# Performance work log

Measured on AMD Instinct MI355X. Metric: run time of the kernel, lower is better.

## Reference

```python
import jax, jax.numpy as jnp
import numpy as np

N_NODES = 100000


def setup_inputs() -> dict:
    key = jax.random.key(0)
    ks = jax.random.split(key, 6)
    x = jax.random.normal(ks[0], (N_NODES, 3), dtype=jnp.float32)
    edge_index = jax.random.randint(ks[1], (2, 1600000), 0, N_NODES, dtype=jnp.int32)
    W1 = jax.random.normal(ks[2], (6, 64), dtype=jnp.float32) * 0.2
    b1 = jnp.zeros((64,), dtype=jnp.float32)
    W2 = jax.random.normal(ks[3], (67, 128), dtype=jnp.float32) * 0.1
    b2 = jnp.zeros((128,), dtype=jnp.float32)
    Wc = jax.random.normal(ks[4], (128, 5), dtype=jnp.float32) * 0.1
    bc = jnp.zeros((5,), dtype=jnp.float32)
    return {"x": x, "edge_index": edge_index, "W1": W1, "b1": b1,
            "W2": W2, "b2": b2, "Wc": Wc, "bc": bc}


def _pointnet_conv(h, rel, src, dst, W, b, n):
    # gather neighbor features, MLP on [h_j, pos_j - pos_i], max-aggregate per node
    msg = jnp.concatenate([h[src], rel], axis=-1) @ W + b  # [E, out]
    agg = jax.ops.segment_max(msg, dst, num_segments=n)    # [N, out]
    return jax.nn.relu(agg)  # relu also maps -inf (isolated nodes) to 0


def reference(x, edge_index, W1, b1, W2, b2, Wc, bc):
    src, dst = edge_index[0], edge_index[1]
    pos = x  # forward uses data.x for both x and pos
    rel = pos[src] - pos[dst]                       # [E, 3]
    h = _pointnet_conv(x, rel, src, dst, W1, b1, N_NODES)   # [N, 64]
    h = _pointnet_conv(h, rel, src, dst, W2, b2, N_NODES)   # [N, 128]
    logits = h @ Wc + bc                            # [N, 5]
    return jax.nn.log_softmax(logits, axis=-1)
```

## Files before the change

### kernel.cpp

```cpp
#include <hip/hip_runtime.h>
#include <cstdint>

#define CAP 56
#define NBITS 7
#define BINSZ 128
#define TILE_E 4096
#define SCANN 1024
#define EPT (TILE_E/256)

typedef _Float16 h2 __attribute__((ext_vector_type(2)));
typedef _Float16 h4 __attribute__((ext_vector_type(4)));
typedef _Float16 h8 __attribute__((ext_vector_type(8)));
typedef float f32x4 __attribute__((ext_vector_type(4)));

static __device__ inline h8 pkmax8(h8 a, h8 b) {
#if __has_builtin(__builtin_elementwise_max)
    return __builtin_elementwise_max(a, b);
#else
    h8 r;
    #pragma unroll
    for (int i = 0; i < 8; i += 2) {
        h2 aa = { a[i], a[i+1] }, bb = { b[i], b[i+1] }, rr;
        asm("v_pk_max_f16 %0, %1, %2" : "=v"(rr) : "v"(aa), "v"(bb));
        r[i] = rr.x; r[i+1] = rr.y;
    }
    return r;
#endif
}

__global__ __launch_bounds__(256) void bin_kernel(
    const float* __restrict__ x, const int* __restrict__ ei,
    float4* __restrict__ xp, int* __restrict__ words_out,
    int* __restrict__ tsc, int N, int E)
{
    for (int n = blockIdx.x * 256 + threadIdx.x; n < N; n += gridDim.x * 256)
        xp[n] = make_float4(x[n*3], x[n*3+1], x[n*3+2], 0.f);

    __shared__ int hist[SCANN];
    __shared__ int sc[SCANN];
    __shared__ int lofs[SCANN];
    __shared__ int words[TILE_E];
    int t = threadIdx.x;
    int tile = blockIdx.x;
    for (int i = t; i < SCANN; i += 256) { hist[i] = 0; lofs[i] = 0; }
    __syncthreads();
    int e0 = tile * TILE_E;
    int s[EPT], d[EPT];
    #pragma unroll
    for (int i = 0; i < EPT; ++i) {
        int e = e0 + t + i * 256;
        bool ok = e < E;
        s[i] = ok ? ei[e] : 0;
        d[i] = ok ? ei[E + e] : -1;
        if (ok) atomicAdd(&hist[d[i] >> NBITS], 1);
    }
    __syncthreads();
    for (int i = t; i < SCANN; i += 256) sc[i] = hist[i];
    __syncthreads();
    for (int off = 1; off < SCANN; off <<= 1) {
        int v[4];
        #pragma unroll
        for (int j = 0; j < 4; ++j) {
            int i = t + j * 256;
            v[j] = (i >= off) ? sc[i - off] : 0;
        }
        __syncthreads();
        #pragma unroll
        for (int j = 0; j < 4; ++j) sc[t + j * 256] += v[j];
        __syncthreads();
    }
    #pragma unroll
    for (int i = 0; i < EPT; ++i) {
        if (d[i] >= 0) {
            int b = d[i] >> NBITS;
            int p = atomicAdd(&lofs[b], 1);
            int slot = (sc[b] - hist[b]) + p;
            words[slot] = s[i] | ((d[i] & (BINSZ - 1)) << 17);
        }
    }
    __syncthreads();
    int* wo = words_out + tile * TILE_E;
    for (int i = t; i < TILE_E; i += 256) wo[i] = words[i];
    int* to = tsc + tile * SCANN;
    for (int i = t; i < SCANN; i += 256) to[i] = sc[i];
}

__global__ __launch_bounds__(256) void scatter2_kernel(
    const int* __restrict__ words, const int* __restrict__ tsc,
    int* __restrict__ cursor, int* __restrict__ bucket,
    int N, int ntiles)
{
    __shared__ int cur[BINSZ];
    __shared__ int lbuck[BINSZ * CAP];
    int t = threadIdx.x;
    int b = blockIdx.x;
    for (int i = t; i < BINSZ; i += 256) cur[i] = 0;
    __syncthreads();
    for (int tt = t; tt < ntiles; tt += 256) {
        int base = tt * SCANN;
        int s0 = (b > 0) ? tsc[base + b - 1] : 0;
        int s1 = tsc[base + b];
        const int* wp = words + tt * TILE_E;
        for (int i = s0; i < s1; ++i) {
            int w = wp[i];
            int p = atomicAdd(&cur[w >> 17], 1);
            if (p < CAP) lbuck[(w >> 17) * CAP + p] = w & 0x1FFFF;
        }
    }
    __syncthreads();
    int nbase = b * BINSZ;
    for (int dl = t; dl < BINSZ; dl += 256) {
        int n = nbase + dl;
        if (n >= N) continue;
        int c = min(cur[dl], CAP);
        int e = (c + 7) & ~7;
        int s0 = (c > 0) ? lbuck[dl * CAP] : 0;
        for (int p = c; p < e; ++p) lbuck[dl * CAP + p] = s0;
        cursor[n] = c;
    }
    __syncthreads();
    int4* dst = (int4*)(bucket + (size_t)nbase * CAP);
    const int4* srcv = (const int4*)lbuck;
    for (int i = t; i < BINSZ * CAP / 4; i += 256) dst[i] = srcv[i];
}

__global__ __launch_bounds__(256) void agg1_gemm_kernel(
    const float4* __restrict__ xp, const int* __restrict__ cursor,
    const int* __restrict__ bucket, const float* __restrict__ W1,
    const float* __restrict__ b1, const float* __restrict__ W2,
    const float* __restrict__ b2, _Float16* __restrict__ u2h, int N)
{
    __shared__ _Float16 h1[64 * 72];
    __shared__ _Float16 w2t[128 * 72];
    int tid = threadIdx.x;
    int n0  = blockIdx.x * 64;
    int sub = tid & 15;
    int ng  = tid >> 4;

    {
        const float4* W2v4 = (const float4*)W2;
        #pragma unroll
        for (int it = 0; it < 8; ++it) {
            int idx = tid + it * 256;
            int k = idx >> 5, c = (idx & 31) * 4;
            float4 w = W2v4[idx];
            w2t[(c+0)*72 + k] = (_Float16)w.x;
            w2t[(c+1)*72 + k] = (_Float16)w.y;
            w2t[(c+2)*72 + k] = (_Float16)w.z;
            w2t[(c+3)*72 + k] = (_Float16)w.w;
        }
    }

    float4 q0 = ((const float4*)(W1 + 0*64))[sub];
    float4 q1 = ((const float4*)(W1 + 1*64))[sub];
    float4 q2 = ((const float4*)(W1 + 2*64))[sub];
    float4 t0 = ((const float4*)(W1 + 3*64))[sub];
    float4 t1 = ((const float4*)(W1 + 4*64))[sub];
    float4 t2 = ((const float4*)(W1 + 5*64))[sub];
    float4 c0 = make_float4(q0.x+t0.x, q0.y+t0.y, q0.z+t0.z, q0.w+t0.w);
    float4 c1 = make_float4(q1.x+t1.x, q1.y+t1.y, q1.z+t1.z, q1.w+t1.w);
    float4 c2 = make_float4(q2.x+t2.x, q2.y+t2.y, q2.z+t2.z, q2.w+t2.w);
    float4 bb = ((const float4*)b1)[sub];

    #pragma unroll
    for (int pass = 0; pass < 4; ++pass) {
        int nl = pass * 16 + ng;
        int n  = n0 + nl;
        float4 m = make_float4(-3e38f, -3e38f, -3e38f, -3e38f);
        int cnt = 0;
        if (n < N) {
            cnt = cursor[n];
            int rounds = (cnt + 7) & ~7;
            const int4* brow4 = (const int4*)(bucket + (size_t)n * CAP);
            int4 ia = brow4[0], ib = brow4[1];
            for (int j0 = 0; j0 < rounds; j0 += 8) {
                int4 na = brow4[(j0 >> 2) + 2];
                int4 nb = brow4[(j0 >> 2) + 3];
                float4 xs[8];
                xs[0] = xp[ia.x]; xs[1] = xp[ia.y]; xs[2] = xp[ia.z]; xs[3] = xp[ia.w];
                xs[4] = xp[ib.x]; xs[5] = xp[ib.y]; xs[6] = xp[ib.z]; xs[7] = xp[ib.w];
                #pragma unroll
                for (int u = 0; u < 8; ++u) {
                    float4 v;
                    v.x = fmaf(xs[u].x, c0.x, fmaf(xs[u].y, c1.x, xs[u].z * c2.x));
                    v.y = fmaf(xs[u].x, c0.y, fmaf(xs[u].y, c1.y, xs[u].z * c2.y));
                    v.z = fmaf(xs[u].x, c0.z, fmaf(xs[u].y, c1.z, xs[u].z * c2.z));
                    v.w = fmaf(xs[u].x, c0.w, fmaf(xs[u].y, c1.w, xs[u].z * c2.w));
                    m.x = fmaxf(m.x, v.x); m.y = fmaxf(m.y, v.y);
                    m.z = fmaxf(m.z, v.z); m.w = fmaxf(m.w, v.w);
                }
                ia = na; ib = nb;
            }
        }
        float4 xd = (n < N) ? xp[n] : make_float4(0.f, 0.f, 0.f, 0.f);
        float v0 = (cnt > 0) ? fmaxf(m.x + bb.x - (xd.x*t0.x + xd.y*t1.x + xd.z*t2.x), 0.f) : 0.f;
        float v1 = (cnt > 0) ? fmaxf(m.y + bb.y - (xd.x*t0.y + xd.y*t1.y + xd.z*t2.y), 0.f) : 0.f;
        float v2 = (cnt > 0) ? fmaxf(m.z + bb.z - (xd.x*t0.z + xd.y*t1.z + xd.z*t2.z), 0.f) : 0.f;
        float v3 = (cnt > 0) ? fmaxf(m.w + bb.w - (xd.x*t0.w + xd.y*t1.w + xd.z*t2.w), 0.f) : 0.f;
        h4 hv;
        hv.x = (_Float16)v0; hv.y = (_Float16)v1;
        hv.z = (_Float16)v2; hv.w = (_Float16)v3;
        *(h4*)&h1[nl * 72 + 4 * sub] = hv;
    }
    __syncthreads();

    int l   = tid & 63;
    int wv  = tid >> 6;
    int r16 = l & 15;
    int g4  = l >> 4;

    f32x4 acc[8];
    #pragma unroll
    for (int ct = 0; ct < 8; ++ct) acc[ct] = (f32x4){0.f, 0.f, 0.f, 0.f};

    h8 a0 = *(const h8*)&h1[(16*wv + r16) * 72 +      8*g4];
    h8 a1 = *(const h8*)&h1[(16*wv + r16) * 72 + 32 + 8*g4];
    #pragma unroll
    for (int ct = 0; ct < 8; ++ct) {
        h8 b0  = *(const h8*)&w2t[(16*ct + r16) * 72 +      8*g4];
        h8 b1f = *(const h8*)&w2t[(16*ct + r16) * 72 + 32 + 8*g4];
        acc[ct] = __builtin_amdgcn_mfma_f32_16x16x32_f16(a0, b0,  acc[ct], 0, 0, 0);
        acc[ct] = __builtin_amdgcn_mfma_f32_16x16x32_f16(a1, b1f, acc[ct], 0, 0, 0);
    }

    float bbv[8], wxv[8], wyv[8], wzv[8];
    #pragma unroll
    for (int ct = 0; ct < 8; ++ct) {
        int col = 16*ct + r16;
        bbv[ct] = b2[col];
        wxv[ct] = W2[64*128 + col];
        wyv[ct] = W2[65*128 + col];
        wzv[ct] = W2[66*128 + col];
    }
    #pragma unroll
    for (int r = 0; r < 4; ++r) {
        int n = n0 + 16*wv + 4*g4 + r;
        if (n < N) {
            float4 xd = xp[n];
            _Float16* orow = u2h + (size_t)n * 128 + r16;
            #pragma unroll
            for (int ct = 0; ct < 8; ++ct) {
                float v = acc[ct][r] + bbv[ct]
                        + xd.x * wxv[ct] + xd.y * wyv[ct] + xd.z * wzv[ct];
                orow[16*ct] = (_Float16)v;
            }
        }
    }
}

__global__ __launch_bounds__(256) void agg2_head_kernel(
    const float* __restrict__ x, const int* __restrict__ cursor,
    const int* __restrict__ bucket, const float* __restrict__ W2,
    const h8* __restrict__ u2v, const float* __restrict__ Wc,
    const float* __restrict__ bc, float* __restrict__ out, int N)
{
    int gid = blockIdx.x * 256 + threadIdx.x;
    int n   = gid >> 4;
    int sub = threadIdx.x & 15;
    if (n >= N) return;
    int cnt = cursor[n];
    int nr = (cnt + 7) >> 3;
    const int4* brow4 = (const int4*)(bucket + (size_t)n * CAP);
    const _Float16 NEG = (_Float16)(-60000.0f);
    h8 hm = { NEG, NEG, NEG, NEG, NEG, NEG, NEG, NEG };
    if (nr > 0) {
        int4 ia = brow4[0], ib = brow4[1];
        h8 v0 = u2v[(size_t)ia.x * 16 + sub];
        h8 v1 = u2v[(size_t)ia.y * 16 + sub];
        h8 v2 = u2v[(size_t)ia.z * 16 + sub];
        h8 v3 = u2v[(size_t)ia.w * 16 + sub];
        h8 v4 = u2v[(size_t)ib.x * 16 + sub];
        h8 v5 = u2v[(size_t)ib.y * 16 + sub];
        h8 v6 = u2v[(size_t)ib.z * 16 + sub];
        h8 v7 = u2v[(size_t)ib.w * 16 + sub];
        int4 na = brow4[2], nb = brow4[3];
        #pragma unroll 2
        for (int r = 1; r < nr; ++r) {
            h8 w0 = u2v[(size_t)na.x * 16 + sub];
            h8 w1 = u2v[(size_t)na.y * 16 + sub];
            h8 w2_ = u2v[(size_t)na.z * 16 + sub];
            h8 w3 = u2v[(size_t)na.w * 16 + sub];
            h8 w4 = u2v[(size_t)nb.x * 16 + sub];
            h8 w5 = u2v[(size_t)nb.y * 16 + sub];
            h8 w6 = u2v[(size_t)nb.z * 16 + sub];
            h8 w7 = u2v[(size_t)nb.w * 16 + sub];
            na = brow4[2*r + 2]; nb = brow4[2*r + 3];
            hm = pkmax8(hm, v0); hm = pkmax8(hm, v1);
            hm = pkmax8(hm, v2); hm = pkmax8(hm, v3);
            hm = pkmax8(hm, v4); hm = pkmax8(hm, v5);
            hm = pkmax8(hm, v6); hm = pkmax8(hm, v7);
            v0 = w0; v1 = w1; v2 = w2_; v3 = w3;
            v4 = w4; v5 = w5; v6 = w6; v7 = w7;
        }
        hm = pkmax8(hm, v0); hm = pkmax8(hm, v1);
        hm = pkmax8(hm, v2); hm = pkmax8(hm, v3);
        hm = pkmax8(hm, v4); hm = pkmax8(hm, v5);
        hm = pkmax8(hm, v6); hm = pkmax8(hm, v7);
    }
    const float4* W2v = (const float4*)W2;
    float4 wa0 = W2v[64*32 + sub*2], wa1 = W2v[64*32 + sub*2 + 1];
    float4 wb0 = W2v[65*32 + sub*2], wb1 = W2v[65*32 + sub*2 + 1];
    float4 wc0 = W2v[66*32 + sub*2], wc1 = W2v[66*32 + sub*2 + 1];
    float x0 = x[n*3], x1 = x[n*3+1], x2 = x[n*3+2];
    float hh[8];
    hh[0] = (cnt > 0) ? fmaxf((float)hm[0] - (x0*wa0.x + x1*wb0.x + x2*wc0.x), 0.f) : 0.f;
    hh[1] = (cnt > 0) ? fmaxf((float)hm[1] - (x0*wa0.y + x1*wb0.y + x2*wc0.y), 0.f) : 0.f;
    hh[2] = (cnt > 0) ? fmaxf((float)hm[2] - (x0*wa0.z + x1*wb0.z + x2*wc0.z), 0.f) : 0.f;
    hh[3] = (cnt > 0) ? fmaxf((float)hm[3] - (x0*wa0.w + x1*wb0.w + x2*wc0.w), 0.f) : 0.f;
    hh[4] = (cnt > 0) ? fmaxf((float)hm[4] - (x0*wa1.x + x1*wb1.x + x2*wc1.x), 0.f) : 0.f;
    hh[5] = (cnt > 0) ? fmaxf((float)hm[5] - (x0*wa1.y + x1*wb1.y + x2*wc1.y), 0.f) : 0.f;
    hh[6] = (cnt > 0) ? fmaxf((float)hm[6] - (x0*wa1.z + x1*wb1.z + x2*wc1.z), 0.f) : 0.f;
    hh[7] = (cnt > 0) ? fmaxf((float)hm[7] - (x0*wa1.w + x1*wb1.w + x2*wc1.w), 0.f) : 0.f;

    int g = sub * 8;
    float l0 = 0.f, l1 = 0.f, l2 = 0.f, l3 = 0.f, l4 = 0.f;
    #pragma unroll
    for (int k = 0; k < 8; ++k) {
        l0 = fmaf(hh[k], Wc[(g+k)*5+0], l0);
        l1 = fmaf(hh[k], Wc[(g+k)*5+1], l1);
        l2 = fmaf(hh[k], Wc[(g+k)*5+2], l2);
        l3 = fmaf(hh[k], Wc[(g+k)*5+3], l3);
        l4 = fmaf(hh[k], Wc[(g+k)*5+4], l4);
    }
    #pragma unroll
    for (int off = 8; off > 0; off >>= 1) {
        l0 += __shfl_xor(l0, off);
        l1 += __shfl_xor(l1, off);
        l2 += __shfl_xor(l2, off);
        l3 += __shfl_xor(l3, off);
        l4 += __shfl_xor(l4, off);
    }
    l0 += bc[0]; l1 += bc[1]; l2 += bc[2]; l3 += bc[3]; l4 += bc[4];
    float mx  = fmaxf(fmaxf(fmaxf(l0, l1), fmaxf(l2, l3)), l4);
    float s   = expf(l0-mx) + expf(l1-mx) + expf(l2-mx) + expf(l3-mx) + expf(l4-mx);
    float lse = mx + logf(s);
    if (sub < 5) {
        float v = (sub == 0) ? l0 : (sub == 1) ? l1 : (sub == 2) ? l2
                : (sub == 3) ? l3 : l4;
        out[n*5 + sub] = v - lse;
    }
}

extern "C" void kernel_launch(void* const* d_in, const int* in_sizes, int n_in,
                              void* d_out, int out_size, void* d_ws, size_t ws_size,
                              hipStream_t stream)
{
    const float* x  = (const float*)d_in[0];
    const int*   ei = (const int*)d_in[1];
    const float* W1 = (const float*)d_in[2];
    const float* b1 = (const float*)d_in[3];
    const float* W2 = (const float*)d_in[4];
    const float* b2 = (const float*)d_in[5];
    const float* Wc = (const float*)d_in[6];
    const float* bc = (const float*)d_in[7];
    float* out = (float*)d_out;

    int N = in_sizes[0] / 3;
    int E = in_sizes[1] / 2;
    int nbins  = (N + BINSZ - 1) / BINSZ;
    int ntiles = (E + TILE_E - 1) / TILE_E;

    char* ws = (char*)d_ws;
    _Float16* u2h   = (_Float16*)(ws);
    float4* xp      = (float4*)(ws + 25600000);
    int*    words   = (int*)   (ws + 27200000);
    int*    tsc     = (int*)   (ws + 33700000);
    int*    bucket  = (int*)   (ws + 36100000);
    int*    cursor  = (int*)   (ws + 58600000);

    bin_kernel<<<ntiles, 256, 0, stream>>>(x, ei, xp, words, tsc, N, E);
    scatter2_kernel<<<nbins, 256, 0, stream>>>(words, tsc, cursor, bucket,
                                               N, ntiles);
    agg1_gemm_kernel<<<(N + 63) / 64, 256, 0, stream>>>(
        xp, cursor, bucket, W1, b1, W2, b2, u2h, N);
    agg2_head_kernel<<<(N * 16 + 255) / 256, 256, 0, stream>>>(
        x, cursor, bucket, W2, (const h8*)u2h, Wc, bc, out, N);
}
```

Baseline: 211.7 us.

## Fuse bucket scatter into layer-1 aggregation kernel using shared-memory neighbor lists

Merges the scatter kernel that builds per-node neighbor buckets with the layer-1 aggregation/GEMM kernel. Each 64-node block now scans its 128-node bin's word segments, keeps only the half it owns, builds the neighbor lists in LDS, writes them out for layer 2, and reads indices directly from LDS for layer-1 aggregation. This drops a kernel launch and the global re-read of bucket/cursor, but every bin's word segments are now scanned twice (once per half-block), and LDS use per block grows, which may lower occupancy.

```diff
diff --git a/kernel.cpp b/kernel.cpp
--- a/kernel.cpp
+++ b/kernel.cpp
@@ -85,57 +85,23 @@
     for (int i = t; i < SCANN; i += 256) to[i] = sc[i];
 }
 
-__global__ __launch_bounds__(256) void scatter2_kernel(
-    const int* __restrict__ words, const int* __restrict__ tsc,
-    int* __restrict__ cursor, int* __restrict__ bucket,
+__global__ __launch_bounds__(256) void scat_agg1_kernel(
+    const float4* __restrict__ xp, const int* __restrict__ words,
+    const int* __restrict__ tsc, const float* __restrict__ W1,
+    const float* __restrict__ b1, const float* __restrict__ W2,
+    const float* __restrict__ b2, int* __restrict__ cursor,
+    int* __restrict__ bucket, _Float16* __restrict__ u2h,
     int N, int ntiles)
 {
-    __shared__ int cur[BINSZ];
-    __shared__ int lbuck[BINSZ * CAP];
-    int t = threadIdx.x;
-    int b = blockIdx.x;
-    for (int i = t; i < BINSZ; i += 256) cur[i] = 0;
-    __syncthreads();
-    for (int tt = t; tt < ntiles; tt += 256) {
-        int base = tt * SCANN;
-        int s0 = (b > 0) ? tsc[base + b - 1] : 0;
-        int s1 = tsc[base + b];
-        const int* wp = words + tt * TILE_E;
-        for (int i = s0; i < s1; ++i) {
-            int w = wp[i];
-            int p = atomicAdd(&cur[w >> 17], 1);
-            if (p < CAP) lbuck[(w >> 17) * CAP + p] = w & 0x1FFFF;
-        }
-    }
-    __syncthreads();
-    int nbase = b * BINSZ;
-    for (int dl = t; dl < BINSZ; dl += 256) {
-        int n = nbase + dl;
-        if (n >= N) continue;
-        int c = min(cur[dl], CAP);
-        int e = (c + 7) & ~7;
-        int s0 = (c > 0) ? lbuck[dl * CAP] : 0;
-        for (int p = c; p < e; ++p) lbuck[dl * CAP + p] = s0;
-        cursor[n] = c;
-    }
-    __syncthreads();
-    int4* dst = (int4*)(bucket + (size_t)nbase * CAP);
-    const int4* srcv = (const int4*)lbuck;
-    for (int i = t; i < BINSZ * CAP / 4; i += 256) dst[i] = srcv[i];
-}
-
-__global__ __launch_bounds__(256) void agg1_gemm_kernel(
-    const float4* __restrict__ xp, const int* __restrict__ cursor,
-    const int* __restrict__ bucket, const float* __restrict__ W1,
-    const float* __restrict__ b1, const float* __restrict__ W2,
-    const float* __restrict__ b2, _Float16* __restrict__ u2h, int N)
-{
+    __shared__ int cur[64];
+    __shared__ int lbuck[64 * CAP];
+    __shared__ _Float16 w2t[128 * 72];
     __shared__ _Float16 h1[64 * 72];
-    __shared__ _Float16 w2t[128 * 72];
     int tid = threadIdx.x;
-    int n0  = blockIdx.x * 64;
-    int sub = tid & 15;
-    int ng  = tid >> 4;
+    int blk = blockIdx.x;
+    int b   = blk >> 1;
+    int hf  = blk & 1;
+    int n0  = blk * 64;
 
     {
         const float4* W2v4 = (const float4*)W2;
@@ -150,7 +116,45 @@
             w2t[(c+3)*72 + k] = (_Float16)w.w;
         }
     }
-
+    if (tid < 64) cur[tid] = 0;
+    __syncthreads();
+
+    for (int tt = tid; tt < ntiles; tt += 256) {
+        int base = tt * SCANN;
+        int s0 = (b > 0) ? tsc[base + b - 1] : 0;
+        int s1 = tsc[base + b];
+        const int* wp = words + tt * TILE_E;
+        for (int i = s0; i < s1; ++i) {
+            int w = wp[i];
+            int dbin = w >> 17;
+            if ((dbin >> 6) == hf) {
+                int p = atomicAdd(&cur[dbin & 63], 1);
+                if (p < CAP) lbuck[(dbin & 63) * CAP + p] = w & 0x1FFFF;
+            }
+        }
+    }
+    __syncthreads();
+    if (tid < 64) {
+        int dl = tid;
+        int n = n0 + dl;
+        if (n < N) {
+            int c = min(cur[dl], CAP);
+            cur[dl] = c;
+            int e = (c + 7) & ~7;
+            int s0 = (c > 0) ? lbuck[dl * CAP] : 0;
+            for (int p = c; p < e; ++p) lbuck[dl * CAP + p] = s0;
+            cursor[n] = c;
+        }
+    }
+    __syncthreads();
+    {
+        int4* dst = (int4*)(bucket + (size_t)n0 * CAP);
+        const int4* srcv = (const int4*)lbuck;
+        for (int i = tid; i < 64 * CAP / 4; i += 256) dst[i] = srcv[i];
+    }
+
+    int sub = tid & 15;
+    int ng  = tid >> 4;
     float4 q0 = ((const float4*)(W1 + 0*64))[sub];
     float4 q1 = ((const float4*)(W1 + 1*64))[sub];
     float4 q2 = ((const float4*)(W1 + 2*64))[sub];
@@ -169,13 +173,12 @@
         float4 m = make_float4(-3e38f, -3e38f, -3e38f, -3e38f);
         int cnt = 0;
         if (n < N) {
-            cnt = cursor[n];
+            cnt = cur[nl];
             int rounds = (cnt + 7) & ~7;
-            const int4* brow4 = (const int4*)(bucket + (size_t)n * CAP);
-            int4 ia = brow4[0], ib = brow4[1];
+            const int* lb = &lbuck[nl * CAP];
             for (int j0 = 0; j0 < rounds; j0 += 8) {
-                int4 na = brow4[(j0 >> 2) + 2];
-                int4 nb = brow4[(j0 >> 2) + 3];
+                int4 ia = *(const int4*)&lb[j0];
+                int4 ib = *(const int4*)&lb[j0 + 4];
                 float4 xs[8];
                 xs[0] = xp[ia.x]; xs[1] = xp[ia.y]; xs[2] = xp[ia.z]; xs[3] = xp[ia.w];
                 xs[4] = xp[ib.x]; xs[5] = xp[ib.y]; xs[6] = xp[ib.z]; xs[7] = xp[ib.w];
@@ -189,7 +192,6 @@
                     m.x = fmaxf(m.x, v.x); m.y = fmaxf(m.y, v.y);
                     m.z = fmaxf(m.z, v.z); m.w = fmaxf(m.w, v.w);
                 }
-                ia = na; ib = nb;
             }
         }
         float4 xd = (n < N) ? xp[n] : make_float4(0.f, 0.f, 0.f, 0.f);
@@ -357,7 +359,6 @@
 
     int N = in_sizes[0] / 3;
     int E = in_sizes[1] / 2;
-    int nbins  = (N + BINSZ - 1) / BINSZ;
     int ntiles = (E + TILE_E - 1) / TILE_E;
 
     char* ws = (char*)d_ws;
@@ -369,10 +370,8 @@
     int*    cursor  = (int*)   (ws + 58600000);
 
     bin_kernel<<<ntiles, 256, 0, stream>>>(x, ei, xp, words, tsc, N, E);
-    scatter2_kernel<<<nbins, 256, 0, stream>>>(words, tsc, cursor, bucket,
-                                               N, ntiles);
-    agg1_gemm_kernel<<<(N + 63) / 64, 256, 0, stream>>>(
-        xp, cursor, bucket, W1, b1, W2, b2, u2h, N);
+    scat_agg1_kernel<<<(N + 63) / 64, 256, 0, stream>>>(
+        xp, words, tsc, W1, b1, W2, b2, cursor, bucket, u2h, N, ntiles);
     agg2_head_kernel<<<(N * 16 + 255) / 256, 256, 0, stream>>>(
         x, cursor, bucket, W2, (const h8*)u2h, Wc, bc, out, N);
 }
```

Measured after the change: 213.6 us. About the same (+0.9%).
